# Performance work log

Hardware: AMD Instinct MI355X
Metric: run time of the kernel (lower is better)

## Reference

```python
import jax, jax.numpy as jnp
from jax import lax
import numpy as np

NODE_COUNT = 4096
BATCH = 128
THRESHOLD = 1.0
DISSIPATION = 0.1
SPARSITY = 0.9
MAX_ITERS = 100


def setup_inputs() -> dict:
    key = jax.random.key(0)
    k_in, k_conn, k_mask, k_w, k_b = jax.random.split(key, 5)
    input_data = jax.random.normal(k_in, (BATCH, NODE_COUNT), dtype=jnp.float32)
    conn = jax.random.normal(k_conn, (NODE_COUNT, NODE_COUNT), dtype=jnp.float32)
    mask = (jax.random.uniform(k_mask, (NODE_COUNT, NODE_COUNT)) > SPARSITY).astype(jnp.float32)
    conn = conn * mask
    conn = conn / (jnp.abs(conn).sum(axis=1, keepdims=True) + 1e-6)
    # input_proj: Linear(node_count, node_count), torch default init scale
    bound = 1.0 / np.sqrt(NODE_COUNT)
    W = jax.random.uniform(k_w, (NODE_COUNT, NODE_COUNT), minval=-bound, maxval=bound, dtype=jnp.float32)
    b = jax.random.uniform(k_b, (NODE_COUNT,), minval=-bound, maxval=bound, dtype=jnp.float32)
    return {"input_data": input_data, "W": W, "b": b, "connections": conn}


def _avalanche(state, connections):
    """Batched avalanche scan with per-sample sticky early-exit (torch break)."""
    B = state.shape[0]
    done0 = jnp.zeros((B,), dtype=bool)
    total0 = jnp.zeros((B,), dtype=state.dtype)

    def step(carry, _):
        state, done, total = carry
        active = (state > THRESHOLD).astype(state.dtype)          # [B, N]
        n_active = active.sum(axis=1)                              # [B]
        new_done = done | (n_active == 0)                          # break condition
        total = total + jnp.where(new_done, 0.0, n_active)
        # propagated = connections @ active  (per sample)
        prop = jnp.einsum('ij,bj->bi', connections, active)        # [B, N]
        new_state = (state * (1.0 - DISSIPATION) + prop * (1.0 - active)) * (1.0 - active)
        state = jnp.where(new_done[:, None], state, new_state)
        return (state, new_done, total), None

    (state, done, total), _ = lax.scan(step, (state, done0, total0), None, length=MAX_ITERS)
    return state, total


def reference(input_data, W, b, connections):
    projected = input_data @ W.T + b                               # [B, N]
    output, sizes = _avalanche(projected, connections)
    max_size = sizes.max()
    return output, max_size
```

## Files before the change

### kernel.cpp

```cpp
#include <hip/hip_runtime.h>

#define N_NODES 4096
#define BATCH 128
#define SPLITK 16
#define GBN 64

typedef _Float16 f16x4 __attribute__((ext_vector_type(4)));
typedef _Float16 f16x8 __attribute__((ext_vector_type(8)));
typedef float f32x4 __attribute__((ext_vector_type(4)));

#if defined(__has_builtin)
#if __has_builtin(__builtin_amdgcn_cvt_f32_fp8) && __has_builtin(__builtin_amdgcn_cvt_pk_fp8_f32)
#define CONN_FP8 1
#endif
#endif
#ifndef CONN_FP8
#define CONN_FP8 0
#endif

#if CONN_FP8
#define CONN_ELEM_BYTES 1
#define CONN_SCALE (1.0f / 256.0f)
#else
#define CONN_ELEM_BYTES 2
#define CONN_SCALE 1.0f
#endif

__device__ __forceinline__ void conn_store(void* out, size_t off, float v) {
#if CONN_FP8
  ((unsigned char*)out)[off] =
      (unsigned char)(__builtin_amdgcn_cvt_pk_fp8_f32(v * 256.0f, 0.0f, 0, false) & 0xff);
#else
  const unsigned int u = __float_as_uint(v);
  ((unsigned short*)out)[off] = (unsigned short)((u + 0x7FFFu + ((u >> 16) & 1u)) >> 16);
#endif
}

__device__ __forceinline__ float4 conn_load4(const void* cT, int j, int t) {
#if CONN_FP8
  const unsigned int c = *(const unsigned int*)((const unsigned char*)cT + ((size_t)j << 12) + t * 4);
  return make_float4(__builtin_amdgcn_cvt_f32_fp8(c, 0), __builtin_amdgcn_cvt_f32_fp8(c, 1),
                     __builtin_amdgcn_cvt_f32_fp8(c, 2), __builtin_amdgcn_cvt_f32_fp8(c, 3));
#else
  const ushort4 c = *(const ushort4*)((const unsigned short*)cT + ((size_t)j << 12) + t * 4);
  return make_float4(__uint_as_float((unsigned int)c.x << 16),
                     __uint_as_float((unsigned int)c.y << 16),
                     __uint_as_float((unsigned int)c.z << 16),
                     __uint_as_float((unsigned int)c.w << 16));
#endif
}

__global__ __launch_bounds__(256) void transpose_conn_kernel(const float* __restrict__ in,
                                                             void* __restrict__ out) {
  __shared__ float tile[32][33];
  const int bx = blockIdx.x, by = blockIdx.y;
  const int tx = threadIdx.x & 31;
  const int ty = threadIdx.x >> 5;
#pragma unroll
  for (int j = 0; j < 4; ++j) {
    const int r = ty + j * 8;
    tile[r][tx] = in[(size_t)(by * 32 + r) * N_NODES + bx * 32 + tx];
  }
  __syncthreads();
#pragma unroll
  for (int j = 0; j < 4; ++j) {
    const int r = ty + j * 8;
    conn_store(out, (size_t)(bx * 32 + r) * N_NODES + by * 32 + tx, tile[tx][r]);
  }
}

template <int NSPLIT>
__global__ __launch_bounds__(256) void proj_gemm_mfma(const float* __restrict__ A,
                                                      const float* __restrict__ W,
                                                      float* __restrict__ P) {
  constexpr int KC = N_NODES / NSPLIT;
  constexpr int PITCH = 40;
  __shared__ alignas(16) _Float16 Ah[128 * PITCH], Al[128 * PITCH];
  __shared__ alignas(16) _Float16 Bh[GBN * PITCH], Bl[GBN * PITCH];

  const int tid = threadIdx.x;
  const int wave = tid >> 6, lane = tid & 63;
  const int wm = wave >> 1, wn = wave & 1;
  const int g = lane >> 4, lrow = lane & 15;
  const int n0 = blockIdx.x * GBN;
  const int kb = blockIdx.y * KC;
  const int scol = (tid & 7) * 4;
  const int srow = tid >> 3;

  const float* Abase = A + (size_t)srow * N_NODES + kb + scol;
  const float* Wbase = W + (size_t)(n0 + srow) * N_NODES + kb + scol;

  f32x4 acc[4][2] = {};

  float4 av[4], wv[2];
#pragma unroll
  for (int r = 0; r < 4; ++r) av[r] = *(const float4*)(Abase + (size_t)(r * 32) * N_NODES);
#pragma unroll
  for (int r = 0; r < 2; ++r) wv[r] = *(const float4*)(Wbase + (size_t)(r * 32) * N_NODES);

  for (int k2 = 0; k2 < KC; k2 += 32) {
    __syncthreads();
#pragma unroll
    for (int r = 0; r < 4; ++r) {
      const int row = srow + r * 32;
      f16x4 hi, lo;
      const float x0 = av[r].x * 256.f, x1 = av[r].y * 256.f,
                  x2 = av[r].z * 256.f, x3 = av[r].w * 256.f;
      hi[0] = (_Float16)x0; lo[0] = (_Float16)(x0 - (float)hi[0]);
      hi[1] = (_Float16)x1; lo[1] = (_Float16)(x1 - (float)hi[1]);
      hi[2] = (_Float16)x2; lo[2] = (_Float16)(x2 - (float)hi[2]);
      hi[3] = (_Float16)x3; lo[3] = (_Float16)(x3 - (float)hi[3]);
      *(f16x4*)&Ah[row * PITCH + scol] = hi;
      *(f16x4*)&Al[row * PITCH + scol] = lo;
    }
#pragma unroll
    for (int r = 0; r < 2; ++r) {
      const int row = srow + r * 32;
      f16x4 hi, lo;
      const float x0 = wv[r].x * 64.f, x1 = wv[r].y * 64.f,
                  x2 = wv[r].z * 64.f, x3 = wv[r].w * 64.f;
      hi[0] = (_Float16)x0; lo[0] = (_Float16)(x0 - (float)hi[0]);
      hi[1] = (_Float16)x1; lo[1] = (_Float16)(x1 - (float)hi[1]);
      hi[2] = (_Float16)x2; lo[2] = (_Float16)(x2 - (float)hi[2]);
      hi[3] = (_Float16)x3; lo[3] = (_Float16)(x3 - (float)hi[3]);
      *(f16x4*)&Bh[row * PITCH + scol] = hi;
      *(f16x4*)&Bl[row * PITCH + scol] = lo;
    }
    __syncthreads();

    const int knext = (k2 + 32) & (KC - 1);
#pragma unroll
    for (int r = 0; r < 4; ++r)
      av[r] = *(const float4*)(Abase + (size_t)(r * 32) * N_NODES + knext);
#pragma unroll
    for (int r = 0; r < 2; ++r)
      wv[r] = *(const float4*)(Wbase + (size_t)(r * 32) * N_NODES + knext);

    f16x8 ah[4], al[4], bh[2], bl[2];
#pragma unroll
    for (int fm = 0; fm < 4; ++fm) {
      const int m = wm * 64 + fm * 16 + lrow;
      ah[fm] = *(const f16x8*)&Ah[m * PITCH + g * 8];
      al[fm] = *(const f16x8*)&Al[m * PITCH + g * 8];
    }
#pragma unroll
    for (int fn = 0; fn < 2; ++fn) {
      const int n = wn * 32 + fn * 16 + lrow;
      bh[fn] = *(const f16x8*)&Bh[n * PITCH + g * 8];
      bl[fn] = *(const f16x8*)&Bl[n * PITCH + g * 8];
    }
#pragma unroll
    for (int fm = 0; fm < 4; ++fm)
#pragma unroll
      for (int fn = 0; fn < 2; ++fn) {
        acc[fm][fn] = __builtin_amdgcn_mfma_f32_16x16x32_f16(ah[fm], bh[fn], acc[fm][fn], 0, 0, 0);
        acc[fm][fn] = __builtin_amdgcn_mfma_f32_16x16x32_f16(ah[fm], bl[fn], acc[fm][fn], 0, 0, 0);
        acc[fm][fn] = __builtin_amdgcn_mfma_f32_16x16x32_f16(al[fm], bh[fn], acc[fm][fn], 0, 0, 0);
      }
  }

  constexpr float INV = 1.0f / 16384.0f;
  float* Pbase = P + (size_t)blockIdx.y * BATCH * N_NODES;
#pragma unroll
  for (int fm = 0; fm < 4; ++fm)
#pragma unroll
    for (int fn = 0; fn < 2; ++fn) {
      const int n = n0 + wn * 32 + fn * 16 + lrow;
#pragma unroll
      for (int reg = 0; reg < 4; ++reg) {
        const int m = wm * 64 + fm * 16 + g * 4 + reg;
        Pbase[(size_t)m * N_NODES + n] = acc[fm][fn][reg] * INV;
      }
    }
}

__global__ __launch_bounds__(256) void proj_gemm_valu(const float* __restrict__ A,
                                                      const float* __restrict__ W,
                                                      float* __restrict__ P) {
  __shared__ float As[16][132];
  __shared__ float Bs[16][68];
  const int tid = threadIdx.x;
  const int n0 = blockIdx.x * 64;
  const int tx = tid & 15, ty = tid >> 4;
  const int arow = tid >> 1, acol = (tid & 1) * 8;
  const int brow = tid >> 2, bcol = (tid & 3) * 4;
  float acc[2][4][4] = {};
  const float* Aptr = A + (size_t)arow * N_NODES + acol;
  const float* Wptr = W + (size_t)(n0 + brow) * N_NODES + bcol;
  for (int k0 = 0; k0 < N_NODES; k0 += 16) {
    const float4 a0 = *(const float4*)(Aptr + k0);
    const float4 a1 = *(const float4*)(Aptr + k0 + 4);
    const float4 bv = *(const float4*)(Wptr + k0);
    __syncthreads();
    As[acol + 0][arow] = a0.x; As[acol + 1][arow] = a0.y;
    As[acol + 2][arow] = a0.z; As[acol + 3][arow] = a0.w;
    As[acol + 4][arow] = a1.x; As[acol + 5][arow] = a1.y;
    As[acol + 6][arow] = a1.z; As[acol + 7][arow] = a1.w;
    Bs[bcol + 0][brow] = bv.x; Bs[bcol + 1][brow] = bv.y;
    Bs[bcol + 2][brow] = bv.z; Bs[bcol + 3][brow] = bv.w;
    __syncthreads();
#pragma unroll
    for (int kk = 0; kk < 16; ++kk) {
      const float4 av0 = *(const float4*)&As[kk][ty * 4];
      const float4 av1 = *(const float4*)&As[kk][64 + ty * 4];
      const float4 bv4 = *(const float4*)&Bs[kk][tx * 4];
      const float am[8] = {av0.x, av0.y, av0.z, av0.w, av1.x, av1.y, av1.z, av1.w};
      const float bn[4] = {bv4.x, bv4.y, bv4.z, bv4.w};
#pragma unroll
      for (int i2 = 0; i2 < 2; ++i2)
#pragma unroll
        for (int i = 0; i < 4; ++i)
#pragma unroll
          for (int j = 0; j < 4; ++j)
            acc[i2][i][j] += am[i2 * 4 + i] * bn[j];
    }
  }
#pragma unroll
  for (int i2 = 0; i2 < 2; ++i2)
#pragma unroll
    for (int i = 0; i < 4; ++i) {
      const int m = i2 * 64 + ty * 4 + i;
      *(float4*)(P + (size_t)m * N_NODES + n0 + tx * 4) =
          make_float4(acc[i2][i][0], acc[i2][i][1], acc[i2][i][2], acc[i2][i][3]);
    }
}

__global__ __launch_bounds__(256) void bias_inplace_kernel(float* __restrict__ P,
                                                           const float* __restrict__ bias) {
  const size_t base = ((size_t)blockIdx.x * 256 + threadIdx.x) * 4;
  const int n = (int)(base & (N_NODES - 1));
  float4 s = *(const float4*)(P + base);
  const float4 bv = *(const float4*)(bias + n);
  s.x += bv.x; s.y += bv.y; s.z += bv.z; s.w += bv.w;
  *(float4*)(P + base) = s;
}

template <int MODE, int NSPLIT>
__global__ __launch_bounds__(1024) void avalanche_kernel(const float* __restrict__ Pin,
                                                         const float* __restrict__ bias,
                                                         const void* __restrict__ connv,
                                                         float* __restrict__ out,
                                                         unsigned int* __restrict__ maxslot) {
  const int b = blockIdx.x;
  const int t = threadIdx.x;
  __shared__ unsigned long long mask[64];
  __shared__ int wincl[64];
  __shared__ int list[N_NODES];

  float4 s;
  if (MODE == 1) {
    const float4 bv = *(const float4*)(bias + t * 4);
    s = bv;
#pragma unroll
    for (int sp = 0; sp < NSPLIT; ++sp) {
      const float4 v = *(const float4*)(Pin + (size_t)sp * BATCH * N_NODES +
                                        (size_t)b * N_NODES + t * 4);
      s.x += v.x; s.y += v.y; s.z += v.z; s.w += v.w;
    }
  } else {
    s = *(const float4*)(Pin + (size_t)b * N_NODES + t * 4);
  }

  float total = 0.0f;

  for (int it = 0; it < 100; ++it) {
    const float v0 = s.x, v1 = s.y, v2 = s.z, v3 = s.w;
    unsigned int bits = 0;
    if (v0 > 1.0f) bits |= 1u;
    if (v1 > 1.0f) bits |= 2u;
    if (v2 > 1.0f) bits |= 4u;
    if (v3 > 1.0f) bits |= 8u;

    __syncthreads();
    if (t < 64) mask[t] = 0ULL;
    __syncthreads();
    if (bits) atomicOr(&mask[t >> 4], (unsigned long long)bits << ((t & 15) * 4));
    __syncthreads();

    if (t < 64) {
      int incl = __popcll(mask[t]);
#pragma unroll
      for (int d = 1; d < 64; d <<= 1) {
        const int y = __shfl_up(incl, d);
        if (t >= d) incl += y;
      }
      wincl[t] = incl;
    }
    __syncthreads();
    const int n = wincl[63];
    if (n == 0) break;
    total += (float)n;

    if (t < 64) {
      unsigned long long m = mask[t];
      int o = wincl[t] - __popcll(m);
      while (m) {
        list[o++] = (t << 6) + __builtin_ctzll(m);
        m &= m - 1;
      }
    }
    __syncthreads();

    float4 a0 = make_float4(0.f, 0.f, 0.f, 0.f), a1 = a0, a2 = a0, a3 = a0;
    if (MODE == 1) {
      int idx = 0;
      for (; idx + 8 <= n; idx += 8) {
        const float4 c0 = conn_load4(connv, list[idx + 0], t);
        const float4 c1 = conn_load4(connv, list[idx + 1], t);
        const float4 c2 = conn_load4(connv, list[idx + 2], t);
        const float4 c3 = conn_load4(connv, list[idx + 3], t);
        const float4 c4 = conn_load4(connv, list[idx + 4], t);
        const float4 c5 = conn_load4(connv, list[idx + 5], t);
        const float4 c6 = conn_load4(connv, list[idx + 6], t);
        const float4 c7 = conn_load4(connv, list[idx + 7], t);
        a0.x += c0.x; a0.y += c0.y; a0.z += c0.z; a0.w += c0.w;
        a1.x += c1.x; a1.y += c1.y; a1.z += c1.z; a1.w += c1.w;
        a2.x += c2.x; a2.y += c2.y; a2.z += c2.z; a2.w += c2.w;
        a3.x += c3.x; a3.y += c3.y; a3.z += c3.z; a3.w += c3.w;
        a0.x += c4.x; a0.y += c4.y; a0.z += c4.z; a0.w += c4.w;
        a1.x += c5.x; a1.y += c5.y; a1.z += c5.z; a1.w += c5.w;
        a2.x += c6.x; a2.y += c6.y; a2.z += c6.z; a2.w += c6.w;
        a3.x += c7.x; a3.y += c7.y; a3.z += c7.z; a3.w += c7.w;
      }
      for (; idx < n; ++idx) {
        const float4 c = conn_load4(connv, list[idx], t);
        a0.x += c.x; a0.y += c.y; a0.z += c.z; a0.w += c.w;
      }
    } else {
      const float* conn = (const float*)connv;
      for (int idx = 0; idx < n; ++idx) {
        const int j = list[idx];
        a0.x += conn[(size_t)(t * 4 + 0) * N_NODES + j];
        a0.y += conn[(size_t)(t * 4 + 1) * N_NODES + j];
        a0.z += conn[(size_t)(t * 4 + 2) * N_NODES + j];
        a0.w += conn[(size_t)(t * 4 + 3) * N_NODES + j];
      }
    }
    const float sc = (MODE == 1) ? CONN_SCALE : 1.0f;
    const float4 acc = make_float4(((a0.x + a1.x) + (a2.x + a3.x)) * sc,
                                   ((a0.y + a1.y) + (a2.y + a3.y)) * sc,
                                   ((a0.z + a1.z) + (a2.z + a3.z)) * sc,
                                   ((a0.w + a1.w) + (a2.w + a3.w)) * sc);

    s.x = (v0 > 1.0f) ? 0.0f : 0.9f * v0 + acc.x;
    s.y = (v1 > 1.0f) ? 0.0f : 0.9f * v1 + acc.y;
    s.z = (v2 > 1.0f) ? 0.0f : 0.9f * v2 + acc.z;
    s.w = (v3 > 1.0f) ? 0.0f : 0.9f * v3 + acc.w;
  }

  *(float4*)(out + (size_t)b * N_NODES + t * 4) = s;
  if (t == 0) atomicMax(maxslot, __float_as_uint(total));
}

extern "C" void kernel_launch(void* const* d_in, const int* in_sizes, int n_in,
                              void* d_out, int out_size, void* d_ws, size_t ws_size,
                              hipStream_t stream) {
  const float* input = (const float*)d_in[0];
  const float* W     = (const float*)d_in[1];
  const float* bias  = (const float*)d_in[2];
  const float* conn  = (const float*)d_in[3];
  float* out = (float*)d_out;

  const size_t connT_bytes = (size_t)N_NODES * N_NODES * CONN_ELEM_BYTES;
  const size_t part_bytes  = (size_t)SPLITK * BATCH * N_NODES * sizeof(float);
  unsigned int* maxslot = (unsigned int*)(out + (size_t)BATCH * N_NODES);

  hipMemsetAsync(maxslot, 0, sizeof(unsigned int), stream);

  if (ws_size >= connT_bytes + part_bytes) {
    void* connT = d_ws;
    float* part = (float*)((char*)d_ws + connT_bytes);
    transpose_conn_kernel<<<dim3(128, 128), 256, 0, stream>>>(conn, connT);
    proj_gemm_mfma<SPLITK><<<dim3(N_NODES / GBN, SPLITK), 256, 0, stream>>>(input, W, part);
    avalanche_kernel<1, SPLITK><<<BATCH, 1024, 0, stream>>>(part, bias, connT, out, maxslot);
  } else {
    proj_gemm_valu<<<dim3(N_NODES / 64, 1), 256, 0, stream>>>(input, W, out);
    bias_inplace_kernel<<<BATCH * N_NODES / 1024, 256, 0, stream>>>(out, bias);
    avalanche_kernel<0, 1><<<BATCH, 1024, 0, stream>>>(out, nullptr, conn, out, maxslot);
  }
}
```

Baseline: 75.79 us.

## Fuse conn transpose and projection GEMM into one launch with double-buffered LDS

Merges the connectivity transpose and the split-K projection GEMM into a single kernel whose blocks are partitioned by index, and drops the separate memset by zeroing the max slot inside the kernel. The GEMM moves to a 32-column tile with split-K 8 and double-buffered shared memory, which removes one barrier per k-step. The transpose now works on 64x64 tiles with vectorised float4 loads and packed 4-element stores. The goal is fewer launches and overlap between the two independent prep phases. The cost is a union shared-memory footprint that may lower occupancy, and the avalanche kernel now sums fewer partials.

```diff
diff --git a/kernel.cpp b/kernel.cpp
--- a/kernel.cpp
+++ b/kernel.cpp
@@ -2,8 +2,13 @@
 
 #define N_NODES 4096
 #define BATCH 128
-#define SPLITK 16
-#define GBN 64
+#define SPLITK 8
+#define GBN 32
+#define PITCH 40
+#define KCHUNK (N_NODES / SPLITK)
+#define NIT (KCHUNK / 32)
+#define GEMM_BLOCKS ((N_NODES / GBN) * SPLITK)
+#define TRANS_BLOCKS (64 * 64)
 
 typedef _Float16 f16x4 __attribute__((ext_vector_type(4)));
 typedef _Float16 f16x8 __attribute__((ext_vector_type(8)));
@@ -26,13 +31,20 @@
 #define CONN_SCALE 1.0f
 #endif
 
-__device__ __forceinline__ void conn_store(void* out, size_t off, float v) {
+__device__ __forceinline__ void conn_store4(void* out, size_t off, float4 v) {
 #if CONN_FP8
-  ((unsigned char*)out)[off] =
-      (unsigned char)(__builtin_amdgcn_cvt_pk_fp8_f32(v * 256.0f, 0.0f, 0, false) & 0xff);
+  unsigned int p = __builtin_amdgcn_cvt_pk_fp8_f32(v.x * 256.0f, v.y * 256.0f, 0, false);
+  p = (unsigned int)__builtin_amdgcn_cvt_pk_fp8_f32(v.z * 256.0f, v.w * 256.0f, (int)p, true);
+  *(unsigned int*)((unsigned char*)out + off) = p;
 #else
-  const unsigned int u = __float_as_uint(v);
-  ((unsigned short*)out)[off] = (unsigned short)((u + 0x7FFFu + ((u >> 16) & 1u)) >> 16);
+  const unsigned int ux = __float_as_uint(v.x), uy = __float_as_uint(v.y);
+  const unsigned int uz = __float_as_uint(v.z), uw = __float_as_uint(v.w);
+  ushort4 u;
+  u.x = (unsigned short)((ux + 0x7FFFu + ((ux >> 16) & 1u)) >> 16);
+  u.y = (unsigned short)((uy + 0x7FFFu + ((uy >> 16) & 1u)) >> 16);
+  u.z = (unsigned short)((uz + 0x7FFFu + ((uz >> 16) & 1u)) >> 16);
+  u.w = (unsigned short)((uw + 0x7FFFu + ((uw >> 16) & 1u)) >> 16);
+  *(ushort4*)((unsigned short*)out + off) = u;
 #endif
 }
 
@@ -50,133 +62,145 @@
 #endif
 }
 
-__global__ __launch_bounds__(256) void transpose_conn_kernel(const float* __restrict__ in,
-                                                             void* __restrict__ out) {
-  __shared__ float tile[32][33];
-  const int bx = blockIdx.x, by = blockIdx.y;
-  const int tx = threadIdx.x & 31;
-  const int ty = threadIdx.x >> 5;
-#pragma unroll
-  for (int j = 0; j < 4; ++j) {
-    const int r = ty + j * 8;
-    tile[r][tx] = in[(size_t)(by * 32 + r) * N_NODES + bx * 32 + tx];
-  }
-  __syncthreads();
-#pragma unroll
-  for (int j = 0; j < 4; ++j) {
-    const int r = ty + j * 8;
-    conn_store(out, (size_t)(bx * 32 + r) * N_NODES + by * 32 + tx, tile[tx][r]);
-  }
-}
-
-template <int NSPLIT>
-__global__ __launch_bounds__(256) void proj_gemm_mfma(const float* __restrict__ A,
-                                                      const float* __restrict__ W,
-                                                      float* __restrict__ P) {
-  constexpr int KC = N_NODES / NSPLIT;
-  constexpr int PITCH = 40;
-  __shared__ alignas(16) _Float16 Ah[128 * PITCH], Al[128 * PITCH];
-  __shared__ alignas(16) _Float16 Bh[GBN * PITCH], Bl[GBN * PITCH];
-
+struct GemmSmem {
+  alignas(16) _Float16 Ah[2][128 * PITCH];
+  alignas(16) _Float16 Al[2][128 * PITCH];
+  alignas(16) _Float16 Bh[2][GBN * PITCH];
+  alignas(16) _Float16 Bl[2][GBN * PITCH];
+};
+struct TransSmem { float tile[64][65]; };
+union PrepSmem { GemmSmem g; TransSmem t; };
+
+__global__ __launch_bounds__(256) void fused_prep_kernel(const float* __restrict__ A,
+                                                         const float* __restrict__ W,
+                                                         const float* __restrict__ conn,
+                                                         float* __restrict__ P,
+                                                         void* __restrict__ connT,
+                                                         unsigned int* __restrict__ maxslot) {
+  __shared__ PrepSmem sm;
   const int tid = threadIdx.x;
-  const int wave = tid >> 6, lane = tid & 63;
-  const int wm = wave >> 1, wn = wave & 1;
-  const int g = lane >> 4, lrow = lane & 15;
-  const int n0 = blockIdx.x * GBN;
-  const int kb = blockIdx.y * KC;
-  const int scol = (tid & 7) * 4;
-  const int srow = tid >> 3;
-
-  const float* Abase = A + (size_t)srow * N_NODES + kb + scol;
-  const float* Wbase = W + (size_t)(n0 + srow) * N_NODES + kb + scol;
-
-  f32x4 acc[4][2] = {};
-
-  float4 av[4], wv[2];
-#pragma unroll
-  for (int r = 0; r < 4; ++r) av[r] = *(const float4*)(Abase + (size_t)(r * 32) * N_NODES);
-#pragma unroll
-  for (int r = 0; r < 2; ++r) wv[r] = *(const float4*)(Wbase + (size_t)(r * 32) * N_NODES);
-
-  for (int k2 = 0; k2 < KC; k2 += 32) {
-    __syncthreads();
-#pragma unroll
-    for (int r = 0; r < 4; ++r) {
-      const int row = srow + r * 32;
-      f16x4 hi, lo;
-      const float x0 = av[r].x * 256.f, x1 = av[r].y * 256.f,
-                  x2 = av[r].z * 256.f, x3 = av[r].w * 256.f;
-      hi[0] = (_Float16)x0; lo[0] = (_Float16)(x0 - (float)hi[0]);
-      hi[1] = (_Float16)x1; lo[1] = (_Float16)(x1 - (float)hi[1]);
-      hi[2] = (_Float16)x2; lo[2] = (_Float16)(x2 - (float)hi[2]);
-      hi[3] = (_Float16)x3; lo[3] = (_Float16)(x3 - (float)hi[3]);
-      *(f16x4*)&Ah[row * PITCH + scol] = hi;
-      *(f16x4*)&Al[row * PITCH + scol] = lo;
-    }
-#pragma unroll
-    for (int r = 0; r < 2; ++r) {
-      const int row = srow + r * 32;
-      f16x4 hi, lo;
-      const float x0 = wv[r].x * 64.f, x1 = wv[r].y * 64.f,
-                  x2 = wv[r].z * 64.f, x3 = wv[r].w * 64.f;
-      hi[0] = (_Float16)x0; lo[0] = (_Float16)(x0 - (float)hi[0]);
-      hi[1] = (_Float16)x1; lo[1] = (_Float16)(x1 - (float)hi[1]);
-      hi[2] = (_Float16)x2; lo[2] = (_Float16)(x2 - (float)hi[2]);
-      hi[3] = (_Float16)x3; lo[3] = (_Float16)(x3 - (float)hi[3]);
-      *(f16x4*)&Bh[row * PITCH + scol] = hi;
-      *(f16x4*)&Bl[row * PITCH + scol] = lo;
-    }
-    __syncthreads();
-
-    const int knext = (k2 + 32) & (KC - 1);
-#pragma unroll
-    for (int r = 0; r < 4; ++r)
-      av[r] = *(const float4*)(Abase + (size_t)(r * 32) * N_NODES + knext);
-#pragma unroll
-    for (int r = 0; r < 2; ++r)
-      wv[r] = *(const float4*)(Wbase + (size_t)(r * 32) * N_NODES + knext);
-
-    f16x8 ah[4], al[4], bh[2], bl[2];
-#pragma unroll
-    for (int fm = 0; fm < 4; ++fm) {
-      const int m = wm * 64 + fm * 16 + lrow;
-      ah[fm] = *(const f16x8*)&Ah[m * PITCH + g * 8];
-      al[fm] = *(const f16x8*)&Al[m * PITCH + g * 8];
-    }
-#pragma unroll
-    for (int fn = 0; fn < 2; ++fn) {
-      const int n = wn * 32 + fn * 16 + lrow;
-      bh[fn] = *(const f16x8*)&Bh[n * PITCH + g * 8];
-      bl[fn] = *(const f16x8*)&Bl[n * PITCH + g * 8];
-    }
+  const int bid = blockIdx.x;
+
+  if (bid < GEMM_BLOCKS) {
+    if (bid == 0 && tid == 0) *maxslot = 0u;
+    const int wave = tid >> 6, lane = tid & 63;
+    const int wm = wave >> 1, wn = wave & 1;
+    const int g = lane >> 4, lrow = lane & 15;
+    const int n0 = (bid & 127) * GBN;
+    const int kb = (bid >> 7) * KCHUNK;
+    const int srow = tid >> 3;
+    const int scol = (tid & 7) * 4;
+
+    const float* Abase = A + (size_t)srow * N_NODES + kb + scol;
+    const float* Wbase = W + (size_t)(n0 + srow) * N_NODES + kb + scol;
+
+    f32x4 acc[4] = {};
+    float4 avA[4], avB[4], wvA, wvB;
+#pragma unroll
+    for (int r = 0; r < 4; ++r) avA[r] = *(const float4*)(Abase + (size_t)(r * 32) * N_NODES);
+    wvA = *(const float4*)Wbase;
+#pragma unroll
+    for (int r = 0; r < 4; ++r) avB[r] = *(const float4*)(Abase + (size_t)(r * 32) * N_NODES + 32);
+    wvB = *(const float4*)(Wbase + 32);
+
+    auto step = [&](float4 (&av)[4], float4& wv, int buf, int it) {
+#pragma unroll
+      for (int r = 0; r < 4; ++r) {
+        const int row = srow + r * 32;
+        f16x4 hi, lo;
+        const float x0 = av[r].x * 256.f, x1 = av[r].y * 256.f,
+                    x2 = av[r].z * 256.f, x3 = av[r].w * 256.f;
+        hi[0] = (_Float16)x0; lo[0] = (_Float16)(x0 - (float)hi[0]);
+        hi[1] = (_Float16)x1; lo[1] = (_Float16)(x1 - (float)hi[1]);
+        hi[2] = (_Float16)x2; lo[2] = (_Float16)(x2 - (float)hi[2]);
+        hi[3] = (_Float16)x3; lo[3] = (_Float16)(x3 - (float)hi[3]);
+        *(f16x4*)&sm.g.Ah[buf][row * PITCH + scol] = hi;
+        *(f16x4*)&sm.g.Al[buf][row * PITCH + scol] = lo;
+      }
+      {
+        f16x4 hi, lo;
+        const float x0 = wv.x * 64.f, x1 = wv.y * 64.f, x2 = wv.z * 64.f, x3 = wv.w * 64.f;
+        hi[0] = (_Float16)x0; lo[0] = (_Float16)(x0 - (float)hi[0]);
+        hi[1] = (_Float16)x1; lo[1] = (_Float16)(x1 - (float)hi[1]);
+        hi[2] = (_Float16)x2; lo[2] = (_Float16)(x2 - (float)hi[2]);
+        hi[3] = (_Float16)x3; lo[3] = (_Float16)(x3 - (float)hi[3]);
+        *(f16x4*)&sm.g.Bh[buf][srow * PITCH + scol] = hi;
+        *(f16x4*)&sm.g.Bl[buf][srow * PITCH + scol] = lo;
+      }
+      const int knext = ((it + 2) * 32) & (KCHUNK - 1);
+#pragma unroll
+      for (int r = 0; r < 4; ++r)
+        av[r] = *(const float4*)(Abase + (size_t)(r * 32) * N_NODES + knext);
+      wv = *(const float4*)(Wbase + knext);
+
+      __syncthreads();
+
+      f16x8 ah[4], al[4], bh, bl;
+#pragma unroll
+      for (int fm = 0; fm < 4; ++fm) {
+        const int m = wm * 64 + fm * 16 + lrow;
+        ah[fm] = *(const f16x8*)&sm.g.Ah[buf][m * PITCH + g * 8];
+        al[fm] = *(const f16x8*)&sm.g.Al[buf][m * PITCH + g * 8];
+      }
+      const int nn = wn * 16 + lrow;
+      bh = *(const f16x8*)&sm.g.Bh[buf][nn * PITCH + g * 8];
+      bl = *(const f16x8*)&sm.g.Bl[buf][nn * PITCH + g * 8];
+#pragma unroll
+      for (int fm = 0; fm < 4; ++fm) {
+        acc[fm] = __builtin_amdgcn_mfma_f32_16x16x32_f16(ah[fm], bh, acc[fm], 0, 0, 0);
+        acc[fm] = __builtin_amdgcn_mfma_f32_16x16x32_f16(ah[fm], bl, acc[fm], 0, 0, 0);
+        acc[fm] = __builtin_amdgcn_mfma_f32_16x16x32_f16(al[fm], bh, acc[fm], 0, 0, 0);
+      }
+    };
+
+#pragma unroll
+    for (int it = 0; it < NIT; it += 2) {
+      step(avA, wvA, 0, it);
+      step(avB, wvB, 1, it + 1);
+    }
+
+    constexpr float INV = 1.0f / 16384.0f;
+    float* Pb = P + (size_t)(bid >> 7) * BATCH * N_NODES;
+    const int n = n0 + wn * 16 + lrow;
 #pragma unroll
     for (int fm = 0; fm < 4; ++fm)
-#pragma unroll
-      for (int fn = 0; fn < 2; ++fn) {
-        acc[fm][fn] = __builtin_amdgcn_mfma_f32_16x16x32_f16(ah[fm], bh[fn], acc[fm][fn], 0, 0, 0);
-        acc[fm][fn] = __builtin_amdgcn_mfma_f32_16x16x32_f16(ah[fm], bl[fn], acc[fm][fn], 0, 0, 0);
-        acc[fm][fn] = __builtin_amdgcn_mfma_f32_16x16x32_f16(al[fm], bh[fn], acc[fm][fn], 0, 0, 0);
-      }
-  }
-
-  constexpr float INV = 1.0f / 16384.0f;
-  float* Pbase = P + (size_t)blockIdx.y * BATCH * N_NODES;
-#pragma unroll
-  for (int fm = 0; fm < 4; ++fm)
-#pragma unroll
-    for (int fn = 0; fn < 2; ++fn) {
-      const int n = n0 + wn * 32 + fn * 16 + lrow;
 #pragma unroll
       for (int reg = 0; reg < 4; ++reg) {
         const int m = wm * 64 + fm * 16 + g * 4 + reg;
-        Pbase[(size_t)m * N_NODES + n] = acc[fm][fn][reg] * INV;
-      }
-    }
+        Pb[(size_t)m * N_NODES + n] = acc[fm][reg] * INV;
+      }
+  } else {
+    const int idx = bid - GEMM_BLOCKS;
+    const int bx = idx & 63, by = idx >> 6;
+    const int tx = tid & 15, ty = tid >> 4;
+#pragma unroll
+    for (int r = 0; r < 4; ++r) {
+      const float4 v =
+          *(const float4*)(conn + (size_t)(by * 64 + ty + 16 * r) * N_NODES + bx * 64 + tx * 4);
+      sm.t.tile[ty + 16 * r][tx * 4 + 0] = v.x;
+      sm.t.tile[ty + 16 * r][tx * 4 + 1] = v.y;
+      sm.t.tile[ty + 16 * r][tx * 4 + 2] = v.z;
+      sm.t.tile[ty + 16 * r][tx * 4 + 3] = v.w;
+    }
+    __syncthreads();
+#pragma unroll
+    for (int r = 0; r < 4; ++r) {
+      const int orow = ty + 16 * r;
+      float4 v;
+      v.x = sm.t.tile[tx * 4 + 0][orow];
+      v.y = sm.t.tile[tx * 4 + 1][orow];
+      v.z = sm.t.tile[tx * 4 + 2][orow];
+      v.w = sm.t.tile[tx * 4 + 3][orow];
+      conn_store4(connT, (size_t)(bx * 64 + orow) * N_NODES + by * 64 + tx * 4, v);
+    }
+  }
 }
 
 __global__ __launch_bounds__(256) void proj_gemm_valu(const float* __restrict__ A,
                                                       const float* __restrict__ W,
-                                                      float* __restrict__ P) {
+                                                      float* __restrict__ P,
+                                                      unsigned int* __restrict__ maxslot) {
+  if (blockIdx.x == 0 && threadIdx.x == 0) *maxslot = 0u;
   __shared__ float As[16][132];
   __shared__ float Bs[16][68];
   const int tid = threadIdx.x;
@@ -365,16 +389,14 @@
   const size_t part_bytes  = (size_t)SPLITK * BATCH * N_NODES * sizeof(float);
   unsigned int* maxslot = (unsigned int*)(out + (size_t)BATCH * N_NODES);
 
-  hipMemsetAsync(maxslot, 0, sizeof(unsigned int), stream);
-
   if (ws_size >= connT_bytes + part_bytes) {
     void* connT = d_ws;
     float* part = (float*)((char*)d_ws + connT_bytes);
-    transpose_conn_kernel<<<dim3(128, 128), 256, 0, stream>>>(conn, connT);
-    proj_gemm_mfma<SPLITK><<<dim3(N_NODES / GBN, SPLITK), 256, 0, stream>>>(input, W, part);
+    fused_prep_kernel<<<GEMM_BLOCKS + TRANS_BLOCKS, 256, 0, stream>>>(input, W, conn, part,
+                                                                      connT, maxslot);
     avalanche_kernel<1, SPLITK><<<BATCH, 1024, 0, stream>>>(part, bias, connT, out, maxslot);
   } else {
-    proj_gemm_valu<<<dim3(N_NODES / 64, 1), 256, 0, stream>>>(input, W, out);
+    proj_gemm_valu<<<dim3(N_NODES / 64, 1), 256, 0, stream>>>(input, W, out, maxslot);
     bias_inplace_kernel<<<BATCH * N_NODES / 1024, 256, 0, stream>>>(out, bias);
     avalanche_kernel<0, 1><<<BATCH, 1024, 0, stream>>>(out, nullptr, conn, out, maxslot);
   }
```

After: 64.36 us. 15.1% less time.
